# Kernel tuning notes

Measured on AMD Instinct MI355X. Metric: run time of the kernel, lower is better.

## Reference

```python
import jax, jax.numpy as jnp
import numpy as np

N_NODE = 100000
D_IN = 256
HEADS = 4
D_HEAD = 64
N_EDGE = 1600000
NEG_SLOPE = 0.2


def setup_inputs() -> dict:
    key = jax.random.key(0)
    ks = jax.random.split(key, 7)
    x = jax.random.normal(ks[0], (1,), dtype=jnp.float32)  # unused by forward (module uses emb.weight)
    edge_index = jax.random.randint(ks[1], (2, N_EDGE), 0, N_NODE, dtype=jnp.int64)
    # xavier-normal-ish scales
    emb_weight = jax.random.normal(ks[2], (N_NODE, D_IN), dtype=jnp.float32) * np.sqrt(2.0 / (N_NODE + D_IN))
    w_scale = np.sqrt(2.0 / (D_IN + HEADS * D_HEAD))
    W_l = jax.random.normal(ks[3], (D_IN, HEADS * D_HEAD), dtype=jnp.float32) * w_scale
    W_r = jax.random.normal(ks[4], (D_IN, HEADS * D_HEAD), dtype=jnp.float32) * w_scale
    att = jax.random.normal(ks[5], (HEADS, D_HEAD), dtype=jnp.float32) * np.sqrt(2.0 / D_HEAD)
    bias = jnp.zeros((D_HEAD,), dtype=jnp.float32)
    return {"x": x, "edge_index": edge_index, "emb_weight": emb_weight,
            "W_l": W_l, "W_r": W_r, "att": att, "bias": bias}


def reference(x, edge_index, emb_weight, W_l, W_r, att, bias):
    N = emb_weight.shape[0]
    # add self loops (PyG GATv2Conv default add_self_loops=True)
    loops = jnp.arange(N, dtype=edge_index.dtype)
    src = jnp.concatenate([edge_index[0], loops])  # source j (messages flow j -> i)
    dst = jnp.concatenate([edge_index[1], loops])  # target i

    # linear transforms: [N, H, C]
    xl = (emb_weight @ W_l).reshape(N, HEADS, D_HEAD)
    xr = (emb_weight @ W_r).reshape(N, HEADS, D_HEAD)

    # GATv2 edge scores: a^T LeakyReLU(x_l[j] + x_r[i])  -> [E, H]
    e = jax.nn.leaky_relu(xl[src] + xr[dst], negative_slope=NEG_SLOPE)
    score = jnp.einsum('ehc,hc->eh', e, att)

    # segment softmax over incoming edges of each dst node
    smax = jax.ops.segment_max(score, dst, num_segments=N)  # [N, H]
    score = jnp.exp(score - smax[dst])
    denom = jax.ops.segment_sum(score, dst, num_segments=N)
    alpha = score / (denom[dst] + 1e-16)  # [E, H]

    # weighted aggregate of x_l[src]
    out = jax.ops.segment_sum(alpha[:, :, None] * xl[src], dst, num_segments=N)  # [N, H, C]
    out = out.mean(axis=1) + bias  # concat=False -> average heads, then bias

    out = jax.nn.elu(out)
    # stack single embedding then mean over dim 1 is identity
    return out
```

## Files before the change

kernel.cpp:

```cpp
#include <hip/hip_runtime.h>
#include <hip/hip_bf16.h>
#include <stdint.h>

#define D_IN 256
#define NEG 0.2f

typedef unsigned short bf16_t;
typedef __attribute__((ext_vector_type(8))) short bfrag;
typedef __attribute__((ext_vector_type(4))) float ffrag;

__device__ __forceinline__ bf16_t f2bf(float f) {
  unsigned int u = __float_as_uint(f);
  unsigned int r = u + 0x7FFFu + ((u >> 16) & 1u);
  return (bf16_t)(r >> 16);
}
__device__ __forceinline__ unsigned int pk2(float a, float b) {
  return (unsigned int)f2bf(a) | ((unsigned int)f2bf(b) << 16);
}
__device__ __forceinline__ void ld4bf(const bf16_t* p, float* f) {
  uint2 u = *(const uint2*)p;
  f[0] = __uint_as_float(u.x << 16);
  f[1] = __uint_as_float(u.x & 0xFFFF0000u);
  f[2] = __uint_as_float(u.y << 16);
  f[3] = __uint_as_float(u.y & 0xFFFF0000u);
}

__global__ __launch_bounds__(256) void k_zero_wt(int* __restrict__ deg, int n, int zb,
                                                 const float* __restrict__ Wl,
                                                 const float* __restrict__ Wr,
                                                 bf16_t* __restrict__ Wt) {
  const int b = blockIdx.x, tid = threadIdx.x;
  if (b < zb) {
    int i = b * 256 + tid;
    if (i < n) deg[i] = 0;
  } else {
    int gid = (b - zb) * 256 + tid;
    int w = gid >> 16;
    int c = (gid >> 8) & 255;
    int k = gid & 255;
    const float* W = w ? Wr : Wl;
    Wt[gid] = f2bf(W[k * 256 + c]);
  }
}

__global__ __launch_bounds__(256) void k_hist_conv(const int* __restrict__ dst, int E,
                                                   int* __restrict__ deg, int* __restrict__ rank,
                                                   int hb,
                                                   const float* __restrict__ emb,
                                                   bf16_t* __restrict__ embh, int n4) {
  const int b = blockIdx.x, tid = threadIdx.x;
  if (b < hb) {
    int e = b * 256 + tid;
    if (e < E) rank[e] = atomicAdd(&deg[dst[e]], 1);
  } else {
    int i = (b - hb) * 256 + tid;
    if (i < n4) {
      float4 f = ((const float4*)emb)[i];
      uint2 o;
      o.x = pk2(f.x, f.y);
      o.y = pk2(f.z, f.w);
      ((uint2*)embh)[i] = o;
    }
  }
}

__global__ __launch_bounds__(256) void k_scanA(const int* __restrict__ deg,
                                               int* __restrict__ offs,
                                               int* __restrict__ bsum, int N) {
  __shared__ int sh[256];
  int t = threadIdx.x;
  int base = blockIdx.x * 1024 + t * 4;
  int v[4];
#pragma unroll
  for (int q = 0; q < 4; q++) v[q] = (base + q < N) ? deg[base + q] : 0;
  int ls = v[0] + v[1] + v[2] + v[3];
  sh[t] = ls;
  __syncthreads();
  for (int ofs = 1; ofs < 256; ofs <<= 1) {
    int x = (t >= ofs) ? sh[t - ofs] : 0;
    __syncthreads();
    sh[t] += x;
    __syncthreads();
  }
  int run = sh[t] - ls;
#pragma unroll
  for (int q = 0; q < 4; q++) {
    if (base + q < N) offs[base + q] = run;
    run += v[q];
  }
  if (t == 255) bsum[blockIdx.x] = sh[255];
}

__global__ __launch_bounds__(128) void k_scanB(int* __restrict__ bsum, int* __restrict__ offs,
                                               int nb, int E, int N) {
  __shared__ int sh[128];
  int t = threadIdx.x;
  int v = (t < nb) ? bsum[t] : 0;
  sh[t] = v;
  __syncthreads();
  for (int ofs = 1; ofs < 128; ofs <<= 1) {
    int x = (t >= ofs) ? sh[t - ofs] : 0;
    __syncthreads();
    sh[t] += x;
    __syncthreads();
  }
  if (t < nb) bsum[t] = sh[t] - v;
  if (t == 0) offs[N] = E;
}

__global__ __launch_bounds__(256) void k_scanC(int* __restrict__ offs,
                                               const int* __restrict__ bsum, int N) {
  int t = threadIdx.x;
  int base = blockIdx.x * 1024 + t * 4;
  int add = bsum[blockIdx.x];
#pragma unroll
  for (int q = 0; q < 4; q++) {
    int i = base + q;
    if (i < N) offs[i] += add;
  }
}

template <bool USEBF>
__global__ __launch_bounds__(256) void k_gemm_scatter(
    const float* __restrict__ emb, const bf16_t* __restrict__ embh,
    const bf16_t* __restrict__ Wt, bf16_t* __restrict__ xl, bf16_t* __restrict__ xr,
    const int* __restrict__ src, const int* __restrict__ dst,
    const int* __restrict__ offs, const int* __restrict__ rank, int* __restrict__ csr,
    int N, int E, int gb) {
  __shared__ bf16_t As[128][40];
  __shared__ bf16_t Bs[128][40];
  const int tid = threadIdx.x;

  if ((int)blockIdx.x >= gb) {
    int e = ((int)blockIdx.x - gb) * 256 + tid;
    if (e < E) {
      int pos = offs[dst[e]] + rank[e];
      csr[pos] = src[e];
    }
    return;
  }

  const int bx = blockIdx.x >> 2, nt = blockIdx.x & 3;
  const int row0 = bx * 128;
  const bf16_t* Wp = Wt + (size_t)(nt >> 1) * 65536;
  bf16_t* dstp = (nt < 2) ? xl : xr;
  const int c0 = (nt & 1) * 128;

  const int wave = tid >> 6, lane = tid & 63;
  const int m0w = (wave & 1) * 64, n0w = (wave >> 1) * 64;
  const int fr = lane & 15;
  const int aq = (lane >> 4) * 8;

  const int srow = tid >> 1, sseg = (tid & 1) * 16;
  const int grow = row0 + srow;
  const bool aok = grow < N;
  const bf16_t* bp = Wp + (size_t)(c0 + srow) * 256 + sseg;

  ffrag acc[4][4];
#pragma unroll
  for (int mi = 0; mi < 4; mi++)
#pragma unroll
    for (int ni = 0; ni < 4; ni++) acc[mi][ni] = (ffrag)0.f;

  for (int k0 = 0; k0 < 256; k0 += 32) {
    uint4 pa0 = make_uint4(0, 0, 0, 0), pa1 = pa0;
    if (USEBF) {
      const bf16_t* ap = embh + (size_t)grow * 256 + sseg;
      if (aok) {
        pa0 = *(const uint4*)(ap + k0);
        pa1 = *(const uint4*)(ap + k0 + 8);
      }
    } else {
      const float* ap = emb + (size_t)grow * 256 + sseg;
      float4 f0 = make_float4(0, 0, 0, 0), f1 = f0, f2 = f0, f3 = f0;
      if (aok) {
        f0 = *(const float4*)(ap + k0);
        f1 = *(const float4*)(ap + k0 + 4);
        f2 = *(const float4*)(ap + k0 + 8);
        f3 = *(const float4*)(ap + k0 + 12);
      }
      pa0.x = pk2(f0.x, f0.y); pa0.y = pk2(f0.z, f0.w);
      pa0.z = pk2(f1.x, f1.y); pa0.w = pk2(f1.z, f1.w);
      pa1.x = pk2(f2.x, f2.y); pa1.y = pk2(f2.z, f2.w);
      pa1.z = pk2(f3.x, f3.y); pa1.w = pk2(f3.z, f3.w);
    }
    uint4 b0 = *(const uint4*)(bp + k0);
    uint4 b1 = *(const uint4*)(bp + k0 + 8);
    __syncthreads();
    *(uint4*)&As[srow][sseg] = pa0;
    *(uint4*)&As[srow][sseg + 8] = pa1;
    *(uint4*)&Bs[srow][sseg] = b0;
    *(uint4*)&Bs[srow][sseg + 8] = b1;
    __syncthreads();

    bfrag af[4], bfv[4];
#pragma unroll
    for (int mi = 0; mi < 4; mi++) af[mi] = *(const bfrag*)&As[m0w + mi * 16 + fr][aq];
#pragma unroll
    for (int ni = 0; ni < 4; ni++) bfv[ni] = *(const bfrag*)&Bs[n0w + ni * 16 + fr][aq];
#pragma unroll
    for (int mi = 0; mi < 4; mi++)
#pragma unroll
      for (int ni = 0; ni < 4; ni++)
        acc[mi][ni] = __builtin_amdgcn_mfma_f32_16x16x32_bf16(af[mi], bfv[ni], acc[mi][ni], 0, 0, 0);
  }

  const int rbase = m0w + (lane >> 4) * 4;
#pragma unroll
  for (int mi = 0; mi < 4; mi++) {
#pragma unroll
    for (int ni = 0; ni < 4; ni++) {
      int col = c0 + n0w + ni * 16 + fr;
#pragma unroll
      for (int r = 0; r < 4; r++) {
        int row = row0 + rbase + mi * 16 + r;
        if (row < N) dstp[(size_t)row * 256 + col] = f2bf(acc[mi][ni][r]);
      }
    }
  }
}

__device__ __forceinline__ float wred16(float p) {
  p += __shfl_xor(p, 1);
  p += __shfl_xor(p, 2);
  p += __shfl_xor(p, 4);
  p += __shfl_xor(p, 8);
  return p;
}
__device__ __forceinline__ float dotleaky(const float* x, const float* xr, const float* av) {
  float p = 0.f;
#pragma unroll
  for (int q = 0; q < 4; q++) {
    float t = x[q] + xr[q];
    t = fmaxf(t, NEG * t);
    p = fmaf(av[q], t, p);
  }
  return p;
}

__global__ __launch_bounds__(256) void k_edge(const bf16_t* __restrict__ xl,
                                              const bf16_t* __restrict__ xr,
                                              const int* __restrict__ offs,
                                              const int* __restrict__ csr,
                                              const float* __restrict__ att,
                                              const float* __restrict__ bias,
                                              float* __restrict__ out, int N) {
  const int wv = threadIdx.x >> 6;
  const int lane = threadIdx.x & 63;
  const int i = blockIdx.x * 4 + wv;
  if (i >= N) return;
  const int cbase = (lane >> 4) * 64 + (lane & 15) * 4;

  const float4 avv = *(const float4*)(att + cbase);
  const float av[4] = {avv.x, avv.y, avv.z, avv.w};
  float xrv[4], xlv[4];
  ld4bf(xr + (size_t)i * 256 + cbase, xrv);
  ld4bf(xl + (size_t)i * 256 + cbase, xlv);

  float s = wred16(dotleaky(xlv, xrv, av));
  float e = __expf(s);
  float d = e;
  float acc[4] = {e * xlv[0], e * xlv[1], e * xlv[2], e * xlv[3]};

  int k = offs[i];
  const int kend = offs[i + 1];

  for (; k + 4 <= kend; k += 4) {
    int j0 = csr[k], j1 = csr[k + 1], j2 = csr[k + 2], j3 = csr[k + 3];
    float x0[4], x1[4], x2[4], x3[4];
    ld4bf(xl + (size_t)j0 * 256 + cbase, x0);
    ld4bf(xl + (size_t)j1 * 256 + cbase, x1);
    ld4bf(xl + (size_t)j2 * 256 + cbase, x2);
    ld4bf(xl + (size_t)j3 * 256 + cbase, x3);
    float p0 = 0.f, p1 = 0.f, p2 = 0.f, p3 = 0.f;
#pragma unroll
    for (int q = 0; q < 4; q++) {
      float t0 = x0[q] + xrv[q], t1 = x1[q] + xrv[q];
      float t2 = x2[q] + xrv[q], t3 = x3[q] + xrv[q];
      t0 = fmaxf(t0, NEG * t0); t1 = fmaxf(t1, NEG * t1);
      t2 = fmaxf(t2, NEG * t2); t3 = fmaxf(t3, NEG * t3);
      p0 = fmaf(av[q], t0, p0); p1 = fmaf(av[q], t1, p1);
      p2 = fmaf(av[q], t2, p2); p3 = fmaf(av[q], t3, p3);
    }
    float e0 = __expf(wred16(p0)), e1 = __expf(wred16(p1));
    float e2 = __expf(wred16(p2)), e3 = __expf(wred16(p3));
    d += (e0 + e1) + (e2 + e3);
#pragma unroll
    for (int q = 0; q < 4; q++)
      acc[q] += fmaf(e0, x0[q], e1 * x1[q]) + fmaf(e2, x2[q], e3 * x3[q]);
  }
  for (; k < kend; ++k) {
    int j = csr[k];
    ld4bf(xl + (size_t)j * 256 + cbase, xlv);
    float ee = __expf(wred16(dotleaky(xlv, xrv, av)));
    d += ee;
#pragma unroll
    for (int q = 0; q < 4; q++) acc[q] = fmaf(ee, xlv[q], acc[q]);
  }

  float inv = 0.25f / d;
  float v[4];
#pragma unroll
  for (int q = 0; q < 4; q++) v[q] = acc[q] * inv;
#pragma unroll
  for (int q = 0; q < 4; q++) {
    v[q] += __shfl_xor(v[q], 16);
    v[q] += __shfl_xor(v[q], 32);
  }
  if ((lane >> 4) == 0) {
    const float4 bq = *(const float4*)(bias + (lane & 15) * 4);
    const float bb[4] = {bq.x, bq.y, bq.z, bq.w};
    float o[4];
#pragma unroll
    for (int q = 0; q < 4; q++) {
      float x = v[q] + bb[q];
      o[q] = x > 0.f ? x : (__expf(x) - 1.f);
    }
    *(float4*)(out + (size_t)i * 64 + (lane & 15) * 4) = make_float4(o[0], o[1], o[2], o[3]);
  }
}

extern "C" void kernel_launch(void* const* d_in, const int* in_sizes, int n_in,
                              void* d_out, int out_size, void* d_ws, size_t ws_size,
                              hipStream_t stream) {
  const int* edge = (const int*)d_in[1];
  const float* emb = (const float*)d_in[2];
  const float* Wl = (const float*)d_in[3];
  const float* Wr = (const float*)d_in[4];
  const float* att = (const float*)d_in[5];
  const float* bias = (const float*)d_in[6];
  float* out = (float*)d_out;

  const int E = in_sizes[1] / 2;
  const int N = in_sizes[2] / D_IN;
  const int* src = edge;
  const int* dst = edge + E;

  const size_t NB = (size_t)N * 256 * 2;
  char* w = (char*)d_ws;
  bf16_t* xl = (bf16_t*)w;  w += NB;
  bf16_t* xr = (bf16_t*)w;  w += NB;
  bf16_t* Wt = (bf16_t*)w;  w += (size_t)2 * 256 * 256 * 2;
  int* offs = (int*)w;      w += ((size_t)N + 64) * 4;
  int* deg = (int*)w;       w += ((size_t)N + 64) * 4;
  int* bsum = (int*)w;      w += 1024;
  int* rank = (int*)w;      w += (size_t)E * 4;
  int* csr = (int*)w;       w += (size_t)E * 4;
  bf16_t* embh = (bf16_t*)w;
  const size_t need_big = (size_t)(w - (char*)d_ws) + NB;
  const bool big = ws_size >= need_big;

  const int nb = (N + 1023) / 1024;
  const int zb = (N + 255) / 256;
  const int hb = (E + 255) / 256;
  const int n4 = big ? N * 64 : 0;
  const int cb = big ? (n4 + 255) / 256 : 0;
  const int gb = ((N + 127) / 128) * 4;
  const int sb = hb;

  hipLaunchKernelGGL(k_zero_wt, dim3(zb + 512), dim3(256), 0, stream, deg, N, zb, Wl, Wr, Wt);
  hipLaunchKernelGGL(k_hist_conv, dim3(hb + cb), dim3(256), 0, stream, dst, E, deg, rank, hb,
                     emb, embh, n4);
  hipLaunchKernelGGL(k_scanA, dim3(nb), dim3(256), 0, stream, deg, offs, bsum, N);
  hipLaunchKernelGGL(k_scanB, dim3(1), dim3(128), 0, stream, bsum, offs, nb, E, N);
  hipLaunchKernelGGL(k_scanC, dim3(nb), dim3(256), 0, stream, offs, bsum, N);
  if (big) {
    hipLaunchKernelGGL(k_gemm_scatter<true>, dim3(gb + sb), dim3(256), 0, stream,
                       emb, embh, Wt, xl, xr, src, dst, offs, rank, csr, N, E, gb);
  } else {
    hipLaunchKernelGGL(k_gemm_scatter<false>, dim3(gb + sb), dim3(256), 0, stream,
                       emb, embh, Wt, xl, xr, src, dst, offs, rank, csr, N, E, gb);
  }
  hipLaunchKernelGGL(k_edge, dim3((N + 3) / 4), dim3(256), 0, stream, xl, xr, offs, csr,
                     att, bias, out, N);
}
```

Measured before the change: 462.8 us.

## Rewrite GATv2 scoring via leaky-relu abs decomposition, precompute per-node att dots, split edges across half-waves

The edge score is rewritten using leaky(t) = 0.6t + 0.4|t|. Per-node linear terms a·xl and a·xr are precomputed in the GEMM epilogue into a small buffer. xl and xr are stored pre-scaled by |att|, so the per-edge dot becomes a signed sum of absolute values, evaluated with exp2. The edge kernel now has each half-wave process half of a node's neighbours with 8-wide bf16 loads and combines the halves at the end; the GEMM also gets an XCD-aware block remap. These changes cut per-edge arithmetic and reduction shuffles, but they add extra bf16 rounding from the scaling and a division by |att| that is unsafe if any att entry is zero.

```diff
diff --git a/kernel.cpp b/kernel.cpp
--- a/kernel.cpp
+++ b/kernel.cpp
@@ -4,6 +4,7 @@
 
 #define D_IN 256
 #define NEG 0.2f
+#define LOG2E 1.44269504f
 
 typedef unsigned short bf16_t;
 typedef __attribute__((ext_vector_type(8))) short bfrag;
@@ -17,12 +18,16 @@
 __device__ __forceinline__ unsigned int pk2(float a, float b) {
   return (unsigned int)f2bf(a) | ((unsigned int)f2bf(b) << 16);
 }
-__device__ __forceinline__ void ld4bf(const bf16_t* p, float* f) {
-  uint2 u = *(const uint2*)p;
+__device__ __forceinline__ void ld8bf(const bf16_t* p, float* f) {
+  uint4 u = *(const uint4*)p;
   f[0] = __uint_as_float(u.x << 16);
   f[1] = __uint_as_float(u.x & 0xFFFF0000u);
   f[2] = __uint_as_float(u.y << 16);
   f[3] = __uint_as_float(u.y & 0xFFFF0000u);
+  f[4] = __uint_as_float(u.z << 16);
+  f[5] = __uint_as_float(u.z & 0xFFFF0000u);
+  f[6] = __uint_as_float(u.w << 16);
+  f[7] = __uint_as_float(u.w & 0xFFFF0000u);
 }
 
 __global__ __launch_bounds__(256) void k_zero_wt(int* __restrict__ deg, int n, int zb,
@@ -126,6 +131,7 @@
     const bf16_t* __restrict__ Wt, bf16_t* __restrict__ xl, bf16_t* __restrict__ xr,
     const int* __restrict__ src, const int* __restrict__ dst,
     const int* __restrict__ offs, const int* __restrict__ rank, int* __restrict__ csr,
+    const float* __restrict__ att, float* __restrict__ blr,
     int N, int E, int gb) {
   __shared__ bf16_t As[128][40];
   __shared__ bf16_t Bs[128][40];
@@ -140,7 +146,13 @@
     return;
   }
 
-  const int bx = blockIdx.x >> 2, nt = blockIdx.x & 3;
+  int g = (int)blockIdx.x;
+  {
+    int xcd = g & 7, slot = g >> 3;
+    int q8 = gb >> 3, r8 = gb & 7;
+    g = (xcd < r8 ? xcd * (q8 + 1) : r8 * (q8 + 1) + (xcd - r8) * q8) + slot;
+  }
+  const int bx = g >> 2, nt = g & 3;
   const int row0 = bx * 128;
   const bf16_t* Wp = Wt + (size_t)(nt >> 1) * 65536;
   bf16_t* dstp = (nt < 2) ? xl : xr;
@@ -206,40 +218,55 @@
   }
 
   const int rbase = m0w + (lane >> 4) * 4;
+
+  const int head = (c0 + n0w) >> 6;
+  float aa[4], absa[4];
+#pragma unroll
+  for (int ni = 0; ni < 4; ni++) {
+    aa[ni] = att[c0 + n0w + ni * 16 + fr];
+    absa[ni] = fabsf(aa[ni]);
+  }
+#pragma unroll
+  for (int mi = 0; mi < 4; mi++) {
+#pragma unroll
+    for (int rr = 0; rr < 4; rr++) {
+      float p = aa[0] * acc[mi][0][rr];
+      p = fmaf(aa[1], acc[mi][1][rr], p);
+      p = fmaf(aa[2], acc[mi][2][rr], p);
+      p = fmaf(aa[3], acc[mi][3][rr], p);
+      p += __shfl_xor(p, 1);
+      p += __shfl_xor(p, 2);
+      p += __shfl_xor(p, 4);
+      p += __shfl_xor(p, 8);
+      int row = row0 + rbase + mi * 16 + rr;
+      if (fr == 0 && row < N) blr[(size_t)row * 8 + (nt >> 1) * 4 + head] = p;
+    }
+  }
+
 #pragma unroll
   for (int mi = 0; mi < 4; mi++) {
 #pragma unroll
     for (int ni = 0; ni < 4; ni++) {
       int col = c0 + n0w + ni * 16 + fr;
 #pragma unroll
-      for (int r = 0; r < 4; r++) {
-        int row = row0 + rbase + mi * 16 + r;
-        if (row < N) dstp[(size_t)row * 256 + col] = f2bf(acc[mi][ni][r]);
+      for (int rr = 0; rr < 4; rr++) {
+        int row = row0 + rbase + mi * 16 + rr;
+        if (row < N) dstp[(size_t)row * 256 + col] = f2bf(acc[mi][ni][rr] * absa[ni]);
       }
     }
   }
 }
 
-__device__ __forceinline__ float wred16(float p) {
+__device__ __forceinline__ float red8(float p) {
   p += __shfl_xor(p, 1);
   p += __shfl_xor(p, 2);
   p += __shfl_xor(p, 4);
-  p += __shfl_xor(p, 8);
   return p;
 }
-__device__ __forceinline__ float dotleaky(const float* x, const float* xr, const float* av) {
-  float p = 0.f;
-#pragma unroll
-  for (int q = 0; q < 4; q++) {
-    float t = x[q] + xr[q];
-    t = fmaxf(t, NEG * t);
-    p = fmaf(av[q], t, p);
-  }
-  return p;
-}
-
-__global__ __launch_bounds__(256) void k_edge(const bf16_t* __restrict__ xl,
-                                              const bf16_t* __restrict__ xr,
+
+__global__ __launch_bounds__(256) void k_edge(const bf16_t* __restrict__ ail,
+                                              const bf16_t* __restrict__ air,
+                                              const float* __restrict__ blr,
                                               const int* __restrict__ offs,
                                               const int* __restrict__ csr,
                                               const float* __restrict__ att,
@@ -249,74 +276,114 @@
   const int lane = threadIdx.x & 63;
   const int i = blockIdx.x * 4 + wv;
   if (i >= N) return;
-  const int cbase = (lane >> 4) * 64 + (lane & 15) * 4;
-
-  const float4 avv = *(const float4*)(att + cbase);
-  const float av[4] = {avv.x, avv.y, avv.z, avv.w};
-  float xrv[4], xlv[4];
-  ld4bf(xr + (size_t)i * 256 + cbase, xrv);
-  ld4bf(xl + (size_t)i * 256 + cbase, xlv);
-
-  float s = wred16(dotleaky(xlv, xrv, av));
-  float e = __expf(s);
-  float d = e;
-  float acc[4] = {e * xlv[0], e * xlv[1], e * xlv[2], e * xlv[3]};
-
-  int k = offs[i];
+  const int half = lane >> 5;
+  const int r = lane & 31;
+  const int head = r >> 3;
+  const int cbase = head * 64 + (r & 7) * 8;
+  const float C4 = 0.4f * LOG2E, C6 = 0.6f * LOG2E;
+
+  float sgn[8];
+  {
+    float4 a0 = *(const float4*)(att + cbase);
+    float4 a1 = *(const float4*)(att + cbase + 4);
+    sgn[0] = copysignf(1.f, a0.x); sgn[1] = copysignf(1.f, a0.y);
+    sgn[2] = copysignf(1.f, a0.z); sgn[3] = copysignf(1.f, a0.w);
+    sgn[4] = copysignf(1.f, a1.x); sgn[5] = copysignf(1.f, a1.y);
+    sgn[6] = copysignf(1.f, a1.z); sgn[7] = copysignf(1.f, a1.w);
+  }
+  float airv[8];
+  ld8bf(air + (size_t)i * 256 + cbase, airv);
+  const float pre_i = C6 * blr[(size_t)i * 8 + 4 + head];
+
+  float d = 0.f;
+  float acc[8] = {0.f, 0.f, 0.f, 0.f, 0.f, 0.f, 0.f, 0.f};
+
+  if (half == 1) {
+    float x[8];
+    ld8bf(ail + (size_t)i * 256 + cbase, x);
+    float p = 0.f;
+#pragma unroll
+    for (int q = 0; q < 8; q++) p = fmaf(sgn[q], fabsf(x[q] + airv[q]), p);
+    p = red8(p);
+    float e = exp2f(fmaf(C4, p, fmaf(C6, blr[(size_t)i * 8 + head], pre_i)));
+    d = e;
+#pragma unroll
+    for (int q = 0; q < 8; q++) acc[q] = e * x[q];
+  }
+
+  const int k0 = offs[i];
   const int kend = offs[i + 1];
-
-  for (; k + 4 <= kend; k += 4) {
-    int j0 = csr[k], j1 = csr[k + 1], j2 = csr[k + 2], j3 = csr[k + 3];
-    float x0[4], x1[4], x2[4], x3[4];
-    ld4bf(xl + (size_t)j0 * 256 + cbase, x0);
-    ld4bf(xl + (size_t)j1 * 256 + cbase, x1);
-    ld4bf(xl + (size_t)j2 * 256 + cbase, x2);
-    ld4bf(xl + (size_t)j3 * 256 + cbase, x3);
-    float p0 = 0.f, p1 = 0.f, p2 = 0.f, p3 = 0.f;
-#pragma unroll
-    for (int q = 0; q < 4; q++) {
-      float t0 = x0[q] + xrv[q], t1 = x1[q] + xrv[q];
-      float t2 = x2[q] + xrv[q], t3 = x3[q] + xrv[q];
-      t0 = fmaxf(t0, NEG * t0); t1 = fmaxf(t1, NEG * t1);
-      t2 = fmaxf(t2, NEG * t2); t3 = fmaxf(t3, NEG * t3);
-      p0 = fmaf(av[q], t0, p0); p1 = fmaf(av[q], t1, p1);
-      p2 = fmaf(av[q], t2, p2); p3 = fmaf(av[q], t3, p3);
-    }
-    float e0 = __expf(wred16(p0)), e1 = __expf(wred16(p1));
-    float e2 = __expf(wred16(p2)), e3 = __expf(wred16(p3));
-    d += (e0 + e1) + (e2 + e3);
-#pragma unroll
-    for (int q = 0; q < 4; q++)
-      acc[q] += fmaf(e0, x0[q], e1 * x1[q]) + fmaf(e2, x2[q], e3 * x3[q]);
-  }
-  for (; k < kend; ++k) {
+  const int kmid = k0 + ((kend - k0 + 1) >> 1);
+  int k = half ? kmid : k0;
+  const int ke = half ? kend : kmid;
+
+  for (; k + 1 < ke; k += 2) {
+    int j0 = csr[k], j1 = csr[k + 1];
+    float x0[8], x1[8];
+    ld8bf(ail + (size_t)j0 * 256 + cbase, x0);
+    ld8bf(ail + (size_t)j1 * 256 + cbase, x1);
+    float bl0 = blr[(size_t)j0 * 8 + head];
+    float bl1 = blr[(size_t)j1 * 8 + head];
+    float p0 = 0.f, p1 = 0.f;
+#pragma unroll
+    for (int q = 0; q < 8; q++) {
+      p0 = fmaf(sgn[q], fabsf(x0[q] + airv[q]), p0);
+      p1 = fmaf(sgn[q], fabsf(x1[q] + airv[q]), p1);
+    }
+    p0 = red8(p0);
+    p1 = red8(p1);
+    float e0 = exp2f(fmaf(C4, p0, fmaf(C6, bl0, pre_i)));
+    float e1 = exp2f(fmaf(C4, p1, fmaf(C6, bl1, pre_i)));
+    d += e0 + e1;
+#pragma unroll
+    for (int q = 0; q < 8; q++) acc[q] += fmaf(e0, x0[q], e1 * x1[q]);
+  }
+  if (k < ke) {
     int j = csr[k];
-    ld4bf(xl + (size_t)j * 256 + cbase, xlv);
-    float ee = __expf(wred16(dotleaky(xlv, xrv, av)));
-    d += ee;
-#pragma unroll
-    for (int q = 0; q < 4; q++) acc[q] = fmaf(ee, xlv[q], acc[q]);
-  }
-
-  float inv = 0.25f / d;
-  float v[4];
-#pragma unroll
-  for (int q = 0; q < 4; q++) v[q] = acc[q] * inv;
-#pragma unroll
-  for (int q = 0; q < 4; q++) {
+    float x[8];
+    ld8bf(ail + (size_t)j * 256 + cbase, x);
+    float p = 0.f;
+#pragma unroll
+    for (int q = 0; q < 8; q++) p = fmaf(sgn[q], fabsf(x[q] + airv[q]), p);
+    p = red8(p);
+    float e = exp2f(fmaf(C4, p, fmaf(C6, blr[(size_t)j * 8 + head], pre_i)));
+    d += e;
+#pragma unroll
+    for (int q = 0; q < 8; q++) acc[q] = fmaf(e, x[q], acc[q]);
+  }
+
+  d += __shfl_xor(d, 32);
+#pragma unroll
+  for (int q = 0; q < 8; q++) acc[q] += __shfl_xor(acc[q], 32);
+
+  float invd = 0.25f / d;
+  float v[8];
+  {
+    float4 a0 = *(const float4*)(att + cbase);
+    float4 a1 = *(const float4*)(att + cbase + 4);
+    float inva[8] = {1.f / fabsf(a0.x), 1.f / fabsf(a0.y), 1.f / fabsf(a0.z), 1.f / fabsf(a0.w),
+                     1.f / fabsf(a1.x), 1.f / fabsf(a1.y), 1.f / fabsf(a1.z), 1.f / fabsf(a1.w)};
+#pragma unroll
+    for (int q = 0; q < 8; q++) v[q] = acc[q] * invd * inva[q];
+  }
+#pragma unroll
+  for (int q = 0; q < 8; q++) {
+    v[q] += __shfl_xor(v[q], 8);
     v[q] += __shfl_xor(v[q], 16);
-    v[q] += __shfl_xor(v[q], 32);
-  }
-  if ((lane >> 4) == 0) {
-    const float4 bq = *(const float4*)(bias + (lane & 15) * 4);
-    const float bb[4] = {bq.x, bq.y, bq.z, bq.w};
-    float o[4];
-#pragma unroll
-    for (int q = 0; q < 4; q++) {
+  }
+  if ((lane >> 3) == 0) {
+    const int cg = lane & 7;
+    const float4 b0 = *(const float4*)(bias + cg * 8);
+    const float4 b1 = *(const float4*)(bias + cg * 8 + 4);
+    const float bb[8] = {b0.x, b0.y, b0.z, b0.w, b1.x, b1.y, b1.z, b1.w};
+    float o[8];
+#pragma unroll
+    for (int q = 0; q < 8; q++) {
       float x = v[q] + bb[q];
       o[q] = x > 0.f ? x : (__expf(x) - 1.f);
     }
-    *(float4*)(out + (size_t)i * 64 + (lane & 15) * 4) = make_float4(o[0], o[1], o[2], o[3]);
+    *(float4*)(out + (size_t)i * 64 + cg * 8) = make_float4(o[0], o[1], o[2], o[3]);
+    *(float4*)(out + (size_t)i * 64 + cg * 8 + 4) = make_float4(o[4], o[5], o[6], o[7]);
   }
 }
 
@@ -346,6 +413,7 @@
   int* bsum = (int*)w;      w += 1024;
   int* rank = (int*)w;      w += (size_t)E * 4;
   int* csr = (int*)w;       w += (size_t)E * 4;
+  float* blr = (float*)w;   w += (size_t)N * 8 * 4;
   bf16_t* embh = (bf16_t*)w;
   const size_t need_big = (size_t)(w - (char*)d_ws) + NB;
   const bool big = ws_size >= need_big;
@@ -366,11 +434,11 @@
   hipLaunchKernelGGL(k_scanC, dim3(nb), dim3(256), 0, stream, offs, bsum, N);
   if (big) {
     hipLaunchKernelGGL(k_gemm_scatter<true>, dim3(gb + sb), dim3(256), 0, stream,
-                       emb, embh, Wt, xl, xr, src, dst, offs, rank, csr, N, E, gb);
+                       emb, embh, Wt, xl, xr, src, dst, offs, rank, csr, att, blr, N, E, gb);
   } else {
     hipLaunchKernelGGL(k_gemm_scatter<false>, dim3(gb + sb), dim3(256), 0, stream,
-                       emb, embh, Wt, xl, xr, src, dst, offs, rank, csr, N, E, gb);
-  }
-  hipLaunchKernelGGL(k_edge, dim3((N + 3) / 4), dim3(256), 0, stream, xl, xr, offs, csr,
+                       emb, embh, Wt, xl, xr, src, dst, offs, rank, csr, att, blr, N, E, gb);
+  }
+  hipLaunchKernelGGL(k_edge, dim3((N + 3) / 4), dim3(256), 0, stream, xl, xr, blr, offs, csr,
                      att, bias, out, N);
 }
```

Result: slower. 520.6 us (+12.5%).

## Fold attention magnitudes into projections and rewrite LeakyReLU score via abs identity

Applied to the files above, without the earlier changes.

The GEMM epilogue scales each xl/xr column by |att|, so the edge kernel only needs the sign of att. LeakyReLU is rewritten as 0.6*(x + K*|x|), and the per-destination xr part of the dot product is precomputed once. The exp then becomes a single exp2 of an fma, and the |att| scaling is undone at the end through 1/|att|. The GEMM blocks are also remapped across XCDs for better L2 locality. This risks division by zero if any att entry is zero, and adds slight numeric differences from storing scaled values in bf16.

```diff
diff --git a/kernel.cpp b/kernel.cpp
--- a/kernel.cpp
+++ b/kernel.cpp
@@ -4,6 +4,7 @@
 
 #define D_IN 256
 #define NEG 0.2f
+#define LOG2E 1.44269504f
 
 typedef unsigned short bf16_t;
 typedef __attribute__((ext_vector_type(8))) short bfrag;
@@ -126,6 +127,7 @@
     const bf16_t* __restrict__ Wt, bf16_t* __restrict__ xl, bf16_t* __restrict__ xr,
     const int* __restrict__ src, const int* __restrict__ dst,
     const int* __restrict__ offs, const int* __restrict__ rank, int* __restrict__ csr,
+    const float* __restrict__ att,
     int N, int E, int gb) {
   __shared__ bf16_t As[128][40];
   __shared__ bf16_t Bs[128][40];
@@ -140,7 +142,13 @@
     return;
   }
 
-  const int bx = blockIdx.x >> 2, nt = blockIdx.x & 3;
+  int g = (int)blockIdx.x;
+  {
+    int xcd = g & 7, slot = g >> 3;
+    int q8 = gb >> 3, r8 = gb & 7;
+    g = (xcd < r8 ? xcd * (q8 + 1) : r8 * (q8 + 1) + (xcd - r8) * q8) + slot;
+  }
+  const int bx = g >> 2, nt = g & 3;
   const int row0 = bx * 128;
   const bf16_t* Wp = Wt + (size_t)(nt >> 1) * 65536;
   bf16_t* dstp = (nt < 2) ? xl : xr;
@@ -206,15 +214,19 @@
   }
 
   const int rbase = m0w + (lane >> 4) * 4;
+
+  float absa[4];
+#pragma unroll
+  for (int ni = 0; ni < 4; ni++) absa[ni] = fabsf(att[c0 + n0w + ni * 16 + fr]);
 #pragma unroll
   for (int mi = 0; mi < 4; mi++) {
 #pragma unroll
     for (int ni = 0; ni < 4; ni++) {
       int col = c0 + n0w + ni * 16 + fr;
 #pragma unroll
-      for (int r = 0; r < 4; r++) {
-        int row = row0 + rbase + mi * 16 + r;
-        if (row < N) dstp[(size_t)row * 256 + col] = f2bf(acc[mi][ni][r]);
+      for (int rr = 0; rr < 4; rr++) {
+        int row = row0 + rbase + mi * 16 + rr;
+        if (row < N) dstp[(size_t)row * 256 + col] = f2bf(acc[mi][ni][rr] * absa[ni]);
       }
     }
   }
@@ -227,19 +239,9 @@
   p += __shfl_xor(p, 8);
   return p;
 }
-__device__ __forceinline__ float dotleaky(const float* x, const float* xr, const float* av) {
-  float p = 0.f;
-#pragma unroll
-  for (int q = 0; q < 4; q++) {
-    float t = x[q] + xr[q];
-    t = fmaxf(t, NEG * t);
-    p = fmaf(av[q], t, p);
-  }
-  return p;
-}
-
-__global__ __launch_bounds__(256) void k_edge(const bf16_t* __restrict__ xl,
-                                              const bf16_t* __restrict__ xr,
+
+__global__ __launch_bounds__(256) void k_edge(const bf16_t* __restrict__ ail,
+                                              const bf16_t* __restrict__ air,
                                               const int* __restrict__ offs,
                                               const int* __restrict__ csr,
                                               const float* __restrict__ att,
@@ -250,17 +252,40 @@
   const int i = blockIdx.x * 4 + wv;
   if (i >= N) return;
   const int cbase = (lane >> 4) * 64 + (lane & 15) * 4;
+  const float K = 0.66666669f;
+  const float C = 0.6f * LOG2E;
 
   const float4 avv = *(const float4*)(att + cbase);
-  const float av[4] = {avv.x, avv.y, avv.z, avv.w};
-  float xrv[4], xlv[4];
-  ld4bf(xr + (size_t)i * 256 + cbase, xrv);
-  ld4bf(xl + (size_t)i * 256 + cbase, xlv);
-
-  float s = wred16(dotleaky(xlv, xrv, av));
-  float e = __expf(s);
-  float d = e;
-  float acc[4] = {e * xlv[0], e * xlv[1], e * xlv[2], e * xlv[3]};
+  const float sg[4] = {copysignf(1.f, avv.x), copysignf(1.f, avv.y),
+                       copysignf(1.f, avv.z), copysignf(1.f, avv.w)};
+
+  float xrv[4];
+  ld4bf(air + (size_t)i * 256 + cbase, xrv);
+
+  float pb = 0.f;
+#pragma unroll
+  for (int q = 0; q < 4; q++) pb = fmaf(sg[q], xrv[q], pb);
+  const float pre = C * wred16(pb);
+
+  const bf16_t* ailc = ail + cbase;
+
+  float d, acc[4];
+  {
+    float x[4];
+    ld4bf(ailc + ((size_t)(unsigned)i << 8), x);
+    float p = 0.f;
+#pragma unroll
+    for (int q = 0; q < 4; q++) {
+      float t = x[q] + xrv[q];
+      float u = fmaf(K, fabsf(t), x[q]);
+      p = fmaf(sg[q], u, p);
+    }
+    p = wred16(p);
+    float e = exp2f(fmaf(C, p, pre));
+    d = e;
+#pragma unroll
+    for (int q = 0; q < 4; q++) acc[q] = e * x[q];
+  }
 
   int k = offs[i];
   const int kend = offs[i + 1];
@@ -268,40 +293,59 @@
   for (; k + 4 <= kend; k += 4) {
     int j0 = csr[k], j1 = csr[k + 1], j2 = csr[k + 2], j3 = csr[k + 3];
     float x0[4], x1[4], x2[4], x3[4];
-    ld4bf(xl + (size_t)j0 * 256 + cbase, x0);
-    ld4bf(xl + (size_t)j1 * 256 + cbase, x1);
-    ld4bf(xl + (size_t)j2 * 256 + cbase, x2);
-    ld4bf(xl + (size_t)j3 * 256 + cbase, x3);
+    ld4bf(ailc + ((size_t)(unsigned)j0 << 8), x0);
+    ld4bf(ailc + ((size_t)(unsigned)j1 << 8), x1);
+    ld4bf(ailc + ((size_t)(unsigned)j2 << 8), x2);
+    ld4bf(ailc + ((size_t)(unsigned)j3 << 8), x3);
     float p0 = 0.f, p1 = 0.f, p2 = 0.f, p3 = 0.f;
 #pragma unroll
     for (int q = 0; q < 4; q++) {
       float t0 = x0[q] + xrv[q], t1 = x1[q] + xrv[q];
       float t2 = x2[q] + xrv[q], t3 = x3[q] + xrv[q];
-      t0 = fmaxf(t0, NEG * t0); t1 = fmaxf(t1, NEG * t1);
-      t2 = fmaxf(t2, NEG * t2); t3 = fmaxf(t3, NEG * t3);
-      p0 = fmaf(av[q], t0, p0); p1 = fmaf(av[q], t1, p1);
-      p2 = fmaf(av[q], t2, p2); p3 = fmaf(av[q], t3, p3);
-    }
-    float e0 = __expf(wred16(p0)), e1 = __expf(wred16(p1));
-    float e2 = __expf(wred16(p2)), e3 = __expf(wred16(p3));
+      float u0 = fmaf(K, fabsf(t0), x0[q]);
+      float u1 = fmaf(K, fabsf(t1), x1[q]);
+      float u2 = fmaf(K, fabsf(t2), x2[q]);
+      float u3 = fmaf(K, fabsf(t3), x3[q]);
+      p0 = fmaf(sg[q], u0, p0); p1 = fmaf(sg[q], u1, p1);
+      p2 = fmaf(sg[q], u2, p2); p3 = fmaf(sg[q], u3, p3);
+    }
+    float e0 = exp2f(fmaf(C, wred16(p0), pre));
+    float e1 = exp2f(fmaf(C, wred16(p1), pre));
+    float e2 = exp2f(fmaf(C, wred16(p2), pre));
+    float e3 = exp2f(fmaf(C, wred16(p3), pre));
     d += (e0 + e1) + (e2 + e3);
 #pragma unroll
-    for (int q = 0; q < 4; q++)
-      acc[q] += fmaf(e0, x0[q], e1 * x1[q]) + fmaf(e2, x2[q], e3 * x3[q]);
+    for (int q = 0; q < 4; q++) {
+      acc[q] = fmaf(e0, x0[q], acc[q]);
+      acc[q] = fmaf(e1, x1[q], acc[q]);
+      acc[q] = fmaf(e2, x2[q], acc[q]);
+      acc[q] = fmaf(e3, x3[q], acc[q]);
+    }
   }
   for (; k < kend; ++k) {
     int j = csr[k];
-    ld4bf(xl + (size_t)j * 256 + cbase, xlv);
-    float ee = __expf(wred16(dotleaky(xlv, xrv, av)));
-    d += ee;
-#pragma unroll
-    for (int q = 0; q < 4; q++) acc[q] = fmaf(ee, xlv[q], acc[q]);
-  }
-
-  float inv = 0.25f / d;
+    float x[4];
+    ld4bf(ailc + ((size_t)(unsigned)j << 8), x);
+    float p = 0.f;
+#pragma unroll
+    for (int q = 0; q < 4; q++) {
+      float t = x[q] + xrv[q];
+      float u = fmaf(K, fabsf(t), x[q]);
+      p = fmaf(sg[q], u, p);
+    }
+    p = wred16(p);
+    float e = exp2f(fmaf(C, p, pre));
+    d += e;
+#pragma unroll
+    for (int q = 0; q < 4; q++) acc[q] = fmaf(e, x[q], acc[q]);
+  }
+
+  const float invd = 0.25f / d;
+  const float inva[4] = {1.f / fabsf(avv.x), 1.f / fabsf(avv.y),
+                         1.f / fabsf(avv.z), 1.f / fabsf(avv.w)};
   float v[4];
 #pragma unroll
-  for (int q = 0; q < 4; q++) v[q] = acc[q] * inv;
+  for (int q = 0; q < 4; q++) v[q] = acc[q] * invd * inva[q];
 #pragma unroll
   for (int q = 0; q < 4; q++) {
     v[q] += __shfl_xor(v[q], 16);
@@ -366,10 +410,10 @@
   hipLaunchKernelGGL(k_scanC, dim3(nb), dim3(256), 0, stream, offs, bsum, N);
   if (big) {
     hipLaunchKernelGGL(k_gemm_scatter<true>, dim3(gb + sb), dim3(256), 0, stream,
-                       emb, embh, Wt, xl, xr, src, dst, offs, rank, csr, N, E, gb);
+                       emb, embh, Wt, xl, xr, src, dst, offs, rank, csr, att, N, E, gb);
   } else {
     hipLaunchKernelGGL(k_gemm_scatter<false>, dim3(gb + sb), dim3(256), 0, stream,
-                       emb, embh, Wt, xl, xr, src, dst, offs, rank, csr, N, E, gb);
+                       emb, embh, Wt, xl, xr, src, dst, offs, rank, csr, att, N, E, gb);
   }
   hipLaunchKernelGGL(k_edge, dim3((N + 3) / 4), dim3(256), 0, stream, xl, xr, offs, csr,
                      att, bias, out, N);
```

Result: no change. 469.5 us (+1.5%).
